# Kernel optimization log

Measured on AMD Instinct MI355X. Metric: run time of the kernel, lower is better.

Reference implementation:

```python
import jax, jax.numpy as jnp
import numpy as np

GRID = 64            # volume_pixel per axis
VOX = 1.0 / GRID     # voxel_physical (unit-cube volume_physical)
CHUNK = 128          # gaussians per scan step


def _voxel_centers():
    # [V,3] centers of voxels of a unit cube, V = GRID**3
    c = (jnp.arange(GRID, dtype=jnp.float32) + 0.5) * VOX
    zz, yy, xx = jnp.meshgrid(c, c, c, indexing='ij')
    return jnp.stack([xx.ravel(), yy.ravel(), zz.ravel()], axis=-1)


def _quat_to_rotmat(q):
    # q: [N,4] (w,x,y,z), normalized -> [N,3,3]
    q = q / jnp.linalg.norm(q, axis=-1, keepdims=True)
    w, x, y, z = q[:, 0], q[:, 1], q[:, 2], q[:, 3]
    return jnp.stack([
        jnp.stack([1 - 2 * (y * y + z * z), 2 * (x * y - w * z), 2 * (x * z + w * y)], -1),
        jnp.stack([2 * (x * y + w * z), 1 - 2 * (x * x + z * z), 2 * (y * z - w * x)], -1),
        jnp.stack([2 * (x * z - w * y), 2 * (y * z + w * x), 1 - 2 * (x * x + y * y)], -1),
    ], axis=-2)


def _voxelize(means3D, densities, scales, rotations):
    N = means3D.shape[0]
    R = _quat_to_rotmat(rotations)                       # [N,3,3]
    inv_s2 = 1.0 / (scales * scales)                     # [N,3]
    # Sigma^{-1} = R diag(1/s^2) R^T
    Sinv = jnp.einsum('nij,nj,nkj->nik', R, inv_s2, R)   # [N,3,3]
    centers = _voxel_centers()                            # [V,3]
    n_chunks = N // CHUNK
    mu_c = means3D.reshape(n_chunks, CHUNK, 3)
    de_c = densities.reshape(n_chunks, CHUNK)
    Si_c = Sinv.reshape(n_chunks, CHUNK, 3, 3)

    def step(vol, xs):
        mu, dens, Si = xs
        d = centers[None, :, :] - mu[:, None, :]                 # [C,V,3]
        qf = jnp.einsum('cvi,cij,cvj->cv', d, Si, d)             # [C,V]
        vol = vol + jnp.sum(dens[:, None] * jnp.exp(-0.5 * qf), axis=0)
        return vol, None

    vol0 = jnp.zeros((GRID ** 3,), dtype=means3D.dtype)
    volume, _ = jax.lax.scan(step, vol0, (mu_c, de_c, Si_c))
    volume = volume.reshape(GRID, GRID, GRID)
    # screen-space-style radius: 3 sigma of the largest axis, in voxels
    radii = jnp.ceil(3.0 * jnp.max(scales, axis=-1) / VOX).astype(jnp.int32)
    return volume, radii


def setup_inputs() -> dict:
    key = jax.random.key(0)
    k1, k2, k3, k4 = jax.random.split(key, 4)
    N = 4096
    means3D = jax.random.uniform(k1, (N, 3), dtype=jnp.float32)                 # in unit cube
    densities = jax.random.uniform(k2, (N,), dtype=jnp.float32)
    scales = jax.random.uniform(k3, (N, 3), dtype=jnp.float32) * 0.05 + 0.01    # 0.6-3.8 voxels
    rotations = jax.random.normal(k4, (N, 4), dtype=jnp.float32)
    return {"means3D": means3D, "densities": densities, "scales": scales, "rotations": rotations}


def reference(means3D, densities, scales, rotations):
    return _voxelize(means3D, densities, scales, rotations)
```

## Files before the change

### kernel.cpp

```cpp
#include <hip/hip_runtime.h>

#define GRIDN 64
#define NVOX (GRIDN * GRIDN * GRIDN)
#define VOXF (1.0f / 64.0f)
#define QCUT 12.0f
#define EXPSCL (-0.72134752044f)

#define WS_CULLA 0
#define WS_CULLB (4 * 4096)
#define WS_REC   (8 * 4096)

__global__ __launch_bounds__(256) void prep_kernel(
    const float* __restrict__ means, const float* __restrict__ dens,
    const float* __restrict__ scales, const float* __restrict__ rots,
    float* __restrict__ ws, float* __restrict__ radii_out, int N)
{
    int i = blockIdx.x * 256 + threadIdx.x;
    if (i >= N) return;

    float qw = rots[i * 4 + 0], qx = rots[i * 4 + 1];
    float qy = rots[i * 4 + 2], qz = rots[i * 4 + 3];
    float inm = rsqrtf(qw * qw + qx * qx + qy * qy + qz * qz);
    qw *= inm; qx *= inm; qy *= inm; qz *= inm;
    float r00 = 1.f - 2.f * (qy * qy + qz * qz);
    float r01 = 2.f * (qx * qy - qw * qz);
    float r02 = 2.f * (qx * qz + qw * qy);
    float r10 = 2.f * (qx * qy + qw * qz);
    float r11 = 1.f - 2.f * (qx * qx + qz * qz);
    float r12 = 2.f * (qy * qz - qw * qx);
    float r20 = 2.f * (qx * qz - qw * qy);
    float r21 = 2.f * (qy * qz + qw * qx);
    float r22 = 1.f - 2.f * (qx * qx + qy * qy);

    float s0 = scales[i * 3 + 0], s1 = scales[i * 3 + 1], s2 = scales[i * 3 + 2];
    float v0 = s0 * s0, v1 = s1 * s1, v2 = s2 * s2;
    float i0 = 1.f / v0, i1 = 1.f / v1, i2 = 1.f / v2;

    float A = (r00 * r00 * i0 + r01 * r01 * i1 + r02 * r02 * i2) * EXPSCL;
    float B = (r10 * r10 * i0 + r11 * r11 * i1 + r12 * r12 * i2) * EXPSCL;
    float C = (r20 * r20 * i0 + r21 * r21 * i1 + r22 * r22 * i2) * EXPSCL;
    float D = (r00 * r10 * i0 + r01 * r11 * i1 + r02 * r12 * i2) * EXPSCL;
    float E = (r00 * r20 * i0 + r01 * r21 * i1 + r02 * r22 * i2) * EXPSCL;
    float F = (r10 * r20 * i0 + r11 * r21 * i1 + r12 * r22 * i2) * EXPSCL;

    float Cxx = r00 * r00 * v0 + r01 * r01 * v1 + r02 * r02 * v2;
    float Cyy = r10 * r10 * v0 + r11 * r11 * v1 + r12 * r12 * v2;
    float Czz = r20 * r20 * v0 + r21 * r21 * v1 + r22 * r22 * v2;

    float de = fmaxf(dens[i], 1e-30f);
    float qeff = fmaxf(QCUT + 2.0f * logf(de), 0.0f);
    float smax2 = fmaxf(v0, fmaxf(v1, v2));

    float mx = means[i * 3 + 0], my = means[i * 3 + 1], mz = means[i * 3 + 2];
    float4 ca; ca.x = mx; ca.y = my; ca.z = mz; ca.w = sqrtf(qeff * Cxx);
    float4 cb; cb.x = sqrtf(qeff * Cyy); cb.y = sqrtf(qeff * Czz);
    cb.z = qeff * smax2; cb.w = 0.f;
    ((float4*)(ws + WS_CULLA))[i] = ca;
    ((float4*)(ws + WS_CULLB))[i] = cb;

    float4* R = (float4*)(ws + WS_REC + (size_t)i * 16);
    float4 w0; w0.x = A; w0.y = B; w0.z = C; w0.w = 2.f * D;
    float4 w1; w1.x = 2.f * E; w1.y = 2.f * F; w1.z = -0.25f / A; w1.w = log2f(de);
    float4 w2; w2.x = mx; w2.y = my; w2.z = mz; w2.w = 0.f;
    R[0] = w0; R[1] = w1; R[2] = w2;

    float m = fmaxf(s0, fmaxf(s1, s2));
    radii_out[i] = ceilf(m * 3.0f * 64.0f);
}

#define BODY8(v0_, v1_, v2_) do {                                             \
    float dy = py - v2_.y, dz = pz - v2_.z;                                   \
    float tt  = fmaf(v1_.y, dy, v0_.z * dz);                                  \
    float qyz = fmaf(v0_.y * dy, dy, fmaf(tt, dz, v1_.w));                    \
    float gx  = fmaf(v0_.w, dy, v1_.x * dz);                                  \
    float dx0 = px - v2_.x;                                                   \
    float dx1 = dx0 + VOXF,        dx2 = dx0 + 2.f * VOXF;                    \
    float dx3 = dx0 + 3.f * VOXF,  dx4 = dx0 + 4.f * VOXF;                    \
    float dx5 = dx0 + 5.f * VOXF,  dx6 = dx0 + 6.f * VOXF;                    \
    float dx7 = dx0 + 7.f * VOXF;                                             \
    accL.x += __builtin_amdgcn_exp2f(fmaf(dx0, fmaf(v0_.x, dx0, gx), qyz));   \
    accL.y += __builtin_amdgcn_exp2f(fmaf(dx1, fmaf(v0_.x, dx1, gx), qyz));   \
    accL.z += __builtin_amdgcn_exp2f(fmaf(dx2, fmaf(v0_.x, dx2, gx), qyz));   \
    accL.w += __builtin_amdgcn_exp2f(fmaf(dx3, fmaf(v0_.x, dx3, gx), qyz));   \
    accH.x += __builtin_amdgcn_exp2f(fmaf(dx4, fmaf(v0_.x, dx4, gx), qyz));   \
    accH.y += __builtin_amdgcn_exp2f(fmaf(dx5, fmaf(v0_.x, dx5, gx), qyz));   \
    accH.z += __builtin_amdgcn_exp2f(fmaf(dx6, fmaf(v0_.x, dx6, gx), qyz));   \
    accH.w += __builtin_amdgcn_exp2f(fmaf(dx7, fmaf(v0_.x, dx7, gx), qyz));   \
} while (0)

__global__ __launch_bounds__(1024, 8) void vox_kernel(
    const float* __restrict__ ws, float* __restrict__ out, int N)
{
    __shared__ unsigned long long cmask[64];
    __shared__ int slist[3072];
    __shared__ float4 plds[16][64];

    const float* rec = ws + WS_REC;
    const int tid = threadIdx.x;
    const int lane = tid & 63, wave = tid >> 6;
    const int t = (blockIdx.x * 341) & 511;
    const int tX = t & 7, tY = (t >> 3) & 7, tZ = t >> 6;
    const int x0 = tX << 3;
    const int y = (tY << 3) + (lane & 7);
    const int z = (tZ << 3) + (lane >> 3);
    const float px = (x0 + 0.5f) * VOXF;
    const float py = (y + 0.5f) * VOXF;
    const float pz = (z + 0.5f) * VOXF;

    const float lox = (x0 + 0.5f) * VOXF,          hix = (x0 + 7.5f) * VOXF;
    const float loy = ((tY << 3) + 0.5f) * VOXF,   hiy = ((tY << 3) + 7.5f) * VOXF;
    const float loz = ((tZ << 3) + 0.5f) * VOXF,   hiz = ((tZ << 3) + 7.5f) * VOXF;

    const int nch = (N + 63) >> 6;
    #pragma unroll
    for (int k = 0; k < 4; ++k) {
        const int c = (k << 4) | wave;
        unsigned long long bal = 0ull;
        if (c < nch) {
            const int gi = (c << 6) + lane;
            const int gc = gi < N ? gi : N - 1;
            float4 ca = ((const float4*)(ws + WS_CULLA))[gc];
            float4 cb = ((const float4*)(ws + WS_CULLB))[gc];
            float cx = fminf(fmaxf(ca.x, lox), hix) - ca.x;
            float cy = fminf(fmaxf(ca.y, loy), hiy) - ca.y;
            float cz = fminf(fmaxf(ca.z, loz), hiz) - ca.z;
            float d2 = fmaf(cx, cx, fmaf(cy, cy, cz * cz));
            bool keep = (gi < N) && (d2 <= cb.z)
                && (ca.x + ca.w >= lox) && (ca.x - ca.w <= hix)
                && (ca.y + cb.x >= loy) && (ca.y - cb.x <= hiy)
                && (ca.z + cb.y >= loz) && (ca.z - cb.y <= hiz);
            bal = __ballot(keep);
        }
        if (lane == 0) cmask[c] = bal;
    }
    __syncthreads();

    unsigned long long mk = cmask[lane];
    int pc = __popcll(mk);
    int incl = pc;
    #pragma unroll
    for (int d = 1; d < 64; d <<= 1) {
        int t2 = __shfl_up(incl, d, 64);
        if (lane >= d) incl += t2;
    }
    const int excl = incl - pc;
    int cnt = __builtin_amdgcn_readlane(incl, 63);
    if (cnt > 3072) cnt = 3072;

    #pragma unroll
    for (int k = 0; k < 4; ++k) {
        const int c = (k << 4) | wave;
        unsigned long long mc = cmask[c];
        if (mc == 0ull) continue;
        int bse = __builtin_amdgcn_readlane(excl, c);
        if ((mc >> lane) & 1ull) {
            int pre = __popcll(mc & ((1ull << lane) - 1ull));
            int pos = bse + pre;
            if (pos < 3072) slist[pos] = (c << 6) + lane;
        }
    }
    __syncthreads();

    float4 accL, accH;
    accL.x = accL.y = accL.z = accL.w = 0.f;
    accH = accL;

    const int beg = (wave * cnt) >> 4;
    const int end = ((wave + 1) * cnt) >> 4;
    for (int base = beg; base < end; base += 64) {
        int src = base + lane;
        int vidx = slist[src < cnt ? src : cnt - 1];
        int m = end - base; if (m > 64) m = 64;
        int j = 0;
        for (; j + 4 <= m; j += 4) {
            int i0 = __builtin_amdgcn_readlane(vidx, j);
            int i1 = __builtin_amdgcn_readlane(vidx, j + 1);
            int i2 = __builtin_amdgcn_readlane(vidx, j + 2);
            int i3 = __builtin_amdgcn_readlane(vidx, j + 3);
            const float4* P0 = (const float4*)(rec + ((size_t)i0 << 4));
            const float4* P1 = (const float4*)(rec + ((size_t)i1 << 4));
            const float4* P2 = (const float4*)(rec + ((size_t)i2 << 4));
            const float4* P3 = (const float4*)(rec + ((size_t)i3 << 4));
            float4 a0 = P0[0], a1 = P0[1], a2 = P0[2];
            float4 b0 = P1[0], b1 = P1[1], b2 = P1[2];
            float4 c0 = P2[0], c1 = P2[1], c2 = P2[2];
            float4 d0 = P3[0], d1 = P3[1], d2 = P3[2];
            BODY8(a0, a1, a2);
            BODY8(b0, b1, b2);
            BODY8(c0, c1, c2);
            BODY8(d0, d1, d2);
        }
        for (; j < m; ++j) {
            int i0 = __builtin_amdgcn_readlane(vidx, j);
            const float4* P0 = (const float4*)(rec + ((size_t)i0 << 4));
            float4 a0 = P0[0], a1 = P0[1], a2 = P0[2];
            BODY8(a0, a1, a2);
        }
    }

    const int v = (z << 12) + (y << 6) + x0;

    plds[wave][lane] = accL;
    __syncthreads();
    if (wave == 0) {
        float4 r = plds[0][lane];
        #pragma unroll
        for (int w = 1; w < 16; ++w) {
            float4 p = plds[w][lane];
            r.x += p.x; r.y += p.y; r.z += p.z; r.w += p.w;
        }
        *(float4*)&out[v] = r;
    }
    __syncthreads();
    plds[wave][lane] = accH;
    __syncthreads();
    if (wave == 0) {
        float4 r = plds[0][lane];
        #pragma unroll
        for (int w = 1; w < 16; ++w) {
            float4 p = plds[w][lane];
            r.x += p.x; r.y += p.y; r.z += p.z; r.w += p.w;
        }
        *(float4*)&out[v + 4] = r;
    }
}

extern "C" void kernel_launch(void* const* d_in, const int* in_sizes, int n_in,
                              void* d_out, int out_size, void* d_ws, size_t ws_size,
                              hipStream_t stream)
{
    const float* means  = (const float*)d_in[0];
    const float* dens   = (const float*)d_in[1];
    const float* scales = (const float*)d_in[2];
    const float* rots   = (const float*)d_in[3];
    float* out = (float*)d_out;
    float* ws  = (float*)d_ws;
    const int N = in_sizes[1];

    prep_kernel<<<(N + 255) / 256, 256, 0, stream>>>(means, dens, scales, rots,
                                                     ws, out + NVOX, N);
    vox_kernel<<<512, 1024, 0, stream>>>(ws, out, N);
}
```

Before: 25.62 us.

## Move per-tile culling into prep kernel and stream tile lists from global

Per-tile culling and list compaction move from the voxel kernel into the prep kernel. The prep kernel now runs 516 blocks: 4 compute the Gaussian records and 512 cull one tile each, recomputing the bounds from the raw inputs, then write a compacted per-tile index list and count to workspace. The voxel kernel reads its list from global memory with scalar loads and no longer needs the shared list or the culling barriers, which frees LDS and shortens its prologue. In exchange, the recomputed bounds are redundant across the 512 tiles, the list cap drops from 3072 to 2048, and per-element index loads from global replace readlane broadcasts.

```diff
diff --git a/kernel.cpp b/kernel.cpp
--- a/kernel.cpp
+++ b/kernel.cpp
@@ -5,67 +5,142 @@
 #define VOXF (1.0f / 64.0f)
 #define QCUT 12.0f
 #define EXPSCL (-0.72134752044f)
-
-#define WS_CULLA 0
-#define WS_CULLB (4 * 4096)
-#define WS_REC   (8 * 4096)
-
-__global__ __launch_bounds__(256) void prep_kernel(
+#define CAP 2048
+
+#define WS_REC 0
+#define WS_TL  (16 * 4096)
+#define WS_CNT (WS_TL + 512 * CAP)
+
+__global__ __launch_bounds__(1024) void prep_kernel(
     const float* __restrict__ means, const float* __restrict__ dens,
     const float* __restrict__ scales, const float* __restrict__ rots,
-    float* __restrict__ ws, float* __restrict__ radii_out, int N)
+    float* __restrict__ rec, int* __restrict__ tilelist, int* __restrict__ cntg,
+    float* __restrict__ radii_out, int N)
 {
-    int i = blockIdx.x * 256 + threadIdx.x;
-    if (i >= N) return;
-
-    float qw = rots[i * 4 + 0], qx = rots[i * 4 + 1];
-    float qy = rots[i * 4 + 2], qz = rots[i * 4 + 3];
-    float inm = rsqrtf(qw * qw + qx * qx + qy * qy + qz * qz);
-    qw *= inm; qx *= inm; qy *= inm; qz *= inm;
-    float r00 = 1.f - 2.f * (qy * qy + qz * qz);
-    float r01 = 2.f * (qx * qy - qw * qz);
-    float r02 = 2.f * (qx * qz + qw * qy);
-    float r10 = 2.f * (qx * qy + qw * qz);
-    float r11 = 1.f - 2.f * (qx * qx + qz * qz);
-    float r12 = 2.f * (qy * qz - qw * qx);
-    float r20 = 2.f * (qx * qz - qw * qy);
-    float r21 = 2.f * (qy * qz + qw * qx);
-    float r22 = 1.f - 2.f * (qx * qx + qy * qy);
-
-    float s0 = scales[i * 3 + 0], s1 = scales[i * 3 + 1], s2 = scales[i * 3 + 2];
-    float v0 = s0 * s0, v1 = s1 * s1, v2 = s2 * s2;
-    float i0 = 1.f / v0, i1 = 1.f / v1, i2 = 1.f / v2;
-
-    float A = (r00 * r00 * i0 + r01 * r01 * i1 + r02 * r02 * i2) * EXPSCL;
-    float B = (r10 * r10 * i0 + r11 * r11 * i1 + r12 * r12 * i2) * EXPSCL;
-    float C = (r20 * r20 * i0 + r21 * r21 * i1 + r22 * r22 * i2) * EXPSCL;
-    float D = (r00 * r10 * i0 + r01 * r11 * i1 + r02 * r12 * i2) * EXPSCL;
-    float E = (r00 * r20 * i0 + r01 * r21 * i1 + r02 * r22 * i2) * EXPSCL;
-    float F = (r10 * r20 * i0 + r11 * r21 * i1 + r12 * r22 * i2) * EXPSCL;
-
-    float Cxx = r00 * r00 * v0 + r01 * r01 * v1 + r02 * r02 * v2;
-    float Cyy = r10 * r10 * v0 + r11 * r11 * v1 + r12 * r12 * v2;
-    float Czz = r20 * r20 * v0 + r21 * r21 * v1 + r22 * r22 * v2;
-
-    float de = fmaxf(dens[i], 1e-30f);
-    float qeff = fmaxf(QCUT + 2.0f * logf(de), 0.0f);
-    float smax2 = fmaxf(v0, fmaxf(v1, v2));
-
-    float mx = means[i * 3 + 0], my = means[i * 3 + 1], mz = means[i * 3 + 2];
-    float4 ca; ca.x = mx; ca.y = my; ca.z = mz; ca.w = sqrtf(qeff * Cxx);
-    float4 cb; cb.x = sqrtf(qeff * Cyy); cb.y = sqrtf(qeff * Czz);
-    cb.z = qeff * smax2; cb.w = 0.f;
-    ((float4*)(ws + WS_CULLA))[i] = ca;
-    ((float4*)(ws + WS_CULLB))[i] = cb;
-
-    float4* R = (float4*)(ws + WS_REC + (size_t)i * 16);
-    float4 w0; w0.x = A; w0.y = B; w0.z = C; w0.w = 2.f * D;
-    float4 w1; w1.x = 2.f * E; w1.y = 2.f * F; w1.z = -0.25f / A; w1.w = log2f(de);
-    float4 w2; w2.x = mx; w2.y = my; w2.z = mz; w2.w = 0.f;
-    R[0] = w0; R[1] = w1; R[2] = w2;
-
-    float m = fmaxf(s0, fmaxf(s1, s2));
-    radii_out[i] = ceilf(m * 3.0f * 64.0f);
+    __shared__ unsigned long long cmask[64];
+    const int b = blockIdx.x;
+    const int tid = threadIdx.x;
+
+    if (b < 4) {
+        const int i = (b << 10) + tid;
+        if (i >= N) return;
+
+        float qw = rots[i * 4 + 0], qx = rots[i * 4 + 1];
+        float qy = rots[i * 4 + 2], qz = rots[i * 4 + 3];
+        float inm = rsqrtf(qw * qw + qx * qx + qy * qy + qz * qz);
+        qw *= inm; qx *= inm; qy *= inm; qz *= inm;
+        float r00 = 1.f - 2.f * (qy * qy + qz * qz);
+        float r01 = 2.f * (qx * qy - qw * qz);
+        float r02 = 2.f * (qx * qz + qw * qy);
+        float r10 = 2.f * (qx * qy + qw * qz);
+        float r11 = 1.f - 2.f * (qx * qx + qz * qz);
+        float r12 = 2.f * (qy * qz - qw * qx);
+        float r20 = 2.f * (qx * qz - qw * qy);
+        float r21 = 2.f * (qy * qz + qw * qx);
+        float r22 = 1.f - 2.f * (qx * qx + qy * qy);
+
+        float s0 = scales[i * 3 + 0], s1 = scales[i * 3 + 1], s2 = scales[i * 3 + 2];
+        float v0 = s0 * s0, v1 = s1 * s1, v2 = s2 * s2;
+        float i0 = 1.f / v0, i1 = 1.f / v1, i2 = 1.f / v2;
+
+        float A = (r00 * r00 * i0 + r01 * r01 * i1 + r02 * r02 * i2) * EXPSCL;
+        float B = (r10 * r10 * i0 + r11 * r11 * i1 + r12 * r12 * i2) * EXPSCL;
+        float C = (r20 * r20 * i0 + r21 * r21 * i1 + r22 * r22 * i2) * EXPSCL;
+        float D = (r00 * r10 * i0 + r01 * r11 * i1 + r02 * r12 * i2) * EXPSCL;
+        float E = (r00 * r20 * i0 + r01 * r21 * i1 + r02 * r22 * i2) * EXPSCL;
+        float F = (r10 * r20 * i0 + r11 * r21 * i1 + r12 * r22 * i2) * EXPSCL;
+
+        float de = fmaxf(dens[i], 1e-30f);
+        float4* R = (float4*)(rec + (size_t)i * 16);
+        float4 w0; w0.x = A; w0.y = B; w0.z = C; w0.w = 2.f * D;
+        float4 w1; w1.x = 2.f * E; w1.y = 2.f * F; w1.z = -0.25f / A; w1.w = log2f(de);
+        float4 w2; w2.x = means[i * 3 + 0]; w2.y = means[i * 3 + 1];
+        w2.z = means[i * 3 + 2]; w2.w = 0.f;
+        R[0] = w0; R[1] = w1; R[2] = w2;
+
+        radii_out[i] = ceilf(fmaxf(s0, fmaxf(s1, s2)) * 3.0f * 64.0f);
+        return;
+    }
+
+    const int tb = b - 4;
+    const int lane = tid & 63, wave = tid >> 6;
+    const int tX = tb & 7, tY = (tb >> 3) & 7, tZ = tb >> 6;
+    const float lox = ((tX << 3) + 0.5f) * VOXF, hix = ((tX << 3) + 7.5f) * VOXF;
+    const float loy = ((tY << 3) + 0.5f) * VOXF, hiy = ((tY << 3) + 7.5f) * VOXF;
+    const float loz = ((tZ << 3) + 0.5f) * VOXF, hiz = ((tZ << 3) + 7.5f) * VOXF;
+
+    const int nch = (N + 63) >> 6;
+    #pragma unroll
+    for (int k = 0; k < 4; ++k) {
+        const int c = (k << 4) | wave;
+        unsigned long long bal = 0ull;
+        if (c < nch) {
+            const int gi = (c << 6) + lane;
+            const int gc = gi < N ? gi : N - 1;
+            float qw = rots[gc * 4 + 0], qx = rots[gc * 4 + 1];
+            float qy = rots[gc * 4 + 2], qz = rots[gc * 4 + 3];
+            float inm = rsqrtf(qw * qw + qx * qx + qy * qy + qz * qz);
+            float w = qw * inm, a = qx * inm, bq = qy * inm, cq = qz * inm;
+            float r00 = 1.f - 2.f * (bq * bq + cq * cq);
+            float r01 = 2.f * (a * bq - w * cq);
+            float r02 = 2.f * (a * cq + w * bq);
+            float r10 = 2.f * (a * bq + w * cq);
+            float r11 = 1.f - 2.f * (a * a + cq * cq);
+            float r12 = 2.f * (bq * cq - w * a);
+            float r20 = 2.f * (a * cq - w * bq);
+            float r21 = 2.f * (bq * cq + w * a);
+            float r22 = 1.f - 2.f * (a * a + bq * bq);
+            float s0 = scales[gc * 3 + 0], s1 = scales[gc * 3 + 1], s2 = scales[gc * 3 + 2];
+            float v0 = s0 * s0, v1 = s1 * s1, v2 = s2 * s2;
+            float Cxx = r00 * r00 * v0 + r01 * r01 * v1 + r02 * r02 * v2;
+            float Cyy = r10 * r10 * v0 + r11 * r11 * v1 + r12 * r12 * v2;
+            float Czz = r20 * r20 * v0 + r21 * r21 * v1 + r22 * r22 * v2;
+            float de = fmaxf(dens[gc], 1e-30f);
+            float qeff = fmaxf(QCUT + 2.0f * logf(de), 0.0f);
+            float rx = sqrtf(qeff * Cxx), ry = sqrtf(qeff * Cyy), rz = sqrtf(qeff * Czz);
+            float sph = qeff * fmaxf(v0, fmaxf(v1, v2));
+            float mx = means[gc * 3 + 0], my = means[gc * 3 + 1], mz = means[gc * 3 + 2];
+
+            float cx = fminf(fmaxf(mx, lox), hix) - mx;
+            float cy = fminf(fmaxf(my, loy), hiy) - my;
+            float cz = fminf(fmaxf(mz, loz), hiz) - mz;
+            float d2 = fmaf(cx, cx, fmaf(cy, cy, cz * cz));
+            bool keep = (gi < N) && (d2 <= sph)
+                && (mx + rx >= lox) && (mx - rx <= hix)
+                && (my + ry >= loy) && (my - ry <= hiy)
+                && (mz + rz >= loz) && (mz - rz <= hiz);
+            bal = __ballot(keep);
+        }
+        if (lane == 0) cmask[c] = bal;
+    }
+    __syncthreads();
+
+    unsigned long long mk = cmask[lane];
+    int pc = __popcll(mk);
+    int incl = pc;
+    #pragma unroll
+    for (int d = 1; d < 64; d <<= 1) {
+        int t2 = __shfl_up(incl, d, 64);
+        if (lane >= d) incl += t2;
+    }
+    const int excl = incl - pc;
+    int cnt = __builtin_amdgcn_readlane(incl, 63);
+    if (cnt > CAP) cnt = CAP;
+
+    int* tl = tilelist + (size_t)tb * CAP;
+    #pragma unroll
+    for (int k = 0; k < 4; ++k) {
+        const int c = (k << 4) | wave;
+        unsigned long long mc = cmask[c];
+        if (mc == 0ull) continue;
+        int bse = __builtin_amdgcn_readlane(excl, c);
+        if ((mc >> lane) & 1ull) {
+            int pre = __popcll(mc & ((1ull << lane) - 1ull));
+            int pos = bse + pre;
+            if (pos < CAP) tl[pos] = (c << 6) + lane;
+        }
+    }
+    if (tid == 0) cntg[tb] = cnt;
 }
 
 #define BODY8(v0_, v1_, v2_) do {                                             \
@@ -89,13 +164,11 @@
 } while (0)
 
 __global__ __launch_bounds__(1024, 8) void vox_kernel(
-    const float* __restrict__ ws, float* __restrict__ out, int N)
+    const float* __restrict__ rec, const int* __restrict__ tilelist,
+    const int* __restrict__ cntg, float* __restrict__ out, int N)
 {
-    __shared__ unsigned long long cmask[64];
-    __shared__ int slist[3072];
     __shared__ float4 plds[16][64];
 
-    const float* rec = ws + WS_REC;
     const int tid = threadIdx.x;
     const int lane = tid & 63, wave = tid >> 6;
     const int t = (blockIdx.x * 341) & 511;
@@ -107,59 +180,8 @@
     const float py = (y + 0.5f) * VOXF;
     const float pz = (z + 0.5f) * VOXF;
 
-    const float lox = (x0 + 0.5f) * VOXF,          hix = (x0 + 7.5f) * VOXF;
-    const float loy = ((tY << 3) + 0.5f) * VOXF,   hiy = ((tY << 3) + 7.5f) * VOXF;
-    const float loz = ((tZ << 3) + 0.5f) * VOXF,   hiz = ((tZ << 3) + 7.5f) * VOXF;
-
-    const int nch = (N + 63) >> 6;
-    #pragma unroll
-    for (int k = 0; k < 4; ++k) {
-        const int c = (k << 4) | wave;
-        unsigned long long bal = 0ull;
-        if (c < nch) {
-            const int gi = (c << 6) + lane;
-            const int gc = gi < N ? gi : N - 1;
-            float4 ca = ((const float4*)(ws + WS_CULLA))[gc];
-            float4 cb = ((const float4*)(ws + WS_CULLB))[gc];
-            float cx = fminf(fmaxf(ca.x, lox), hix) - ca.x;
-            float cy = fminf(fmaxf(ca.y, loy), hiy) - ca.y;
-            float cz = fminf(fmaxf(ca.z, loz), hiz) - ca.z;
-            float d2 = fmaf(cx, cx, fmaf(cy, cy, cz * cz));
-            bool keep = (gi < N) && (d2 <= cb.z)
-                && (ca.x + ca.w >= lox) && (ca.x - ca.w <= hix)
-                && (ca.y + cb.x >= loy) && (ca.y - cb.x <= hiy)
-                && (ca.z + cb.y >= loz) && (ca.z - cb.y <= hiz);
-            bal = __ballot(keep);
-        }
-        if (lane == 0) cmask[c] = bal;
-    }
-    __syncthreads();
-
-    unsigned long long mk = cmask[lane];
-    int pc = __popcll(mk);
-    int incl = pc;
-    #pragma unroll
-    for (int d = 1; d < 64; d <<= 1) {
-        int t2 = __shfl_up(incl, d, 64);
-        if (lane >= d) incl += t2;
-    }
-    const int excl = incl - pc;
-    int cnt = __builtin_amdgcn_readlane(incl, 63);
-    if (cnt > 3072) cnt = 3072;
-
-    #pragma unroll
-    for (int k = 0; k < 4; ++k) {
-        const int c = (k << 4) | wave;
-        unsigned long long mc = cmask[c];
-        if (mc == 0ull) continue;
-        int bse = __builtin_amdgcn_readlane(excl, c);
-        if ((mc >> lane) & 1ull) {
-            int pre = __popcll(mc & ((1ull << lane) - 1ull));
-            int pos = bse + pre;
-            if (pos < 3072) slist[pos] = (c << 6) + lane;
-        }
-    }
-    __syncthreads();
+    const int cnt = cntg[t];
+    const int* tl = tilelist + (size_t)t * CAP;
 
     float4 accL, accH;
     accL.x = accL.y = accL.z = accL.w = 0.f;
@@ -167,35 +189,27 @@
 
     const int beg = (wave * cnt) >> 4;
     const int end = ((wave + 1) * cnt) >> 4;
-    for (int base = beg; base < end; base += 64) {
-        int src = base + lane;
-        int vidx = slist[src < cnt ? src : cnt - 1];
-        int m = end - base; if (m > 64) m = 64;
-        int j = 0;
-        for (; j + 4 <= m; j += 4) {
-            int i0 = __builtin_amdgcn_readlane(vidx, j);
-            int i1 = __builtin_amdgcn_readlane(vidx, j + 1);
-            int i2 = __builtin_amdgcn_readlane(vidx, j + 2);
-            int i3 = __builtin_amdgcn_readlane(vidx, j + 3);
-            const float4* P0 = (const float4*)(rec + ((size_t)i0 << 4));
-            const float4* P1 = (const float4*)(rec + ((size_t)i1 << 4));
-            const float4* P2 = (const float4*)(rec + ((size_t)i2 << 4));
-            const float4* P3 = (const float4*)(rec + ((size_t)i3 << 4));
-            float4 a0 = P0[0], a1 = P0[1], a2 = P0[2];
-            float4 b0 = P1[0], b1 = P1[1], b2 = P1[2];
-            float4 c0 = P2[0], c1 = P2[1], c2 = P2[2];
-            float4 d0 = P3[0], d1 = P3[1], d2 = P3[2];
-            BODY8(a0, a1, a2);
-            BODY8(b0, b1, b2);
-            BODY8(c0, c1, c2);
-            BODY8(d0, d1, d2);
-        }
-        for (; j < m; ++j) {
-            int i0 = __builtin_amdgcn_readlane(vidx, j);
-            const float4* P0 = (const float4*)(rec + ((size_t)i0 << 4));
-            float4 a0 = P0[0], a1 = P0[1], a2 = P0[2];
-            BODY8(a0, a1, a2);
-        }
+    int p = beg;
+    for (; p + 4 <= end; p += 4) {
+        int i0 = tl[p], i1 = tl[p + 1], i2 = tl[p + 2], i3 = tl[p + 3];
+        const float4* P0 = (const float4*)(rec + ((size_t)i0 << 4));
+        const float4* P1 = (const float4*)(rec + ((size_t)i1 << 4));
+        const float4* P2 = (const float4*)(rec + ((size_t)i2 << 4));
+        const float4* P3 = (const float4*)(rec + ((size_t)i3 << 4));
+        float4 a0 = P0[0], a1 = P0[1], a2 = P0[2];
+        float4 b0 = P1[0], b1 = P1[1], b2 = P1[2];
+        float4 c0 = P2[0], c1 = P2[1], c2 = P2[2];
+        float4 d0 = P3[0], d1 = P3[1], d2 = P3[2];
+        BODY8(a0, a1, a2);
+        BODY8(b0, b1, b2);
+        BODY8(c0, c1, c2);
+        BODY8(d0, d1, d2);
+    }
+    for (; p < end; ++p) {
+        int i0 = tl[p];
+        const float4* P0 = (const float4*)(rec + ((size_t)i0 << 4));
+        float4 a0 = P0[0], a1 = P0[1], a2 = P0[2];
+        BODY8(a0, a1, a2);
     }
 
     const int v = (z << 12) + (y << 6) + x0;
@@ -206,8 +220,8 @@
         float4 r = plds[0][lane];
         #pragma unroll
         for (int w = 1; w < 16; ++w) {
-            float4 p = plds[w][lane];
-            r.x += p.x; r.y += p.y; r.z += p.z; r.w += p.w;
+            float4 q = plds[w][lane];
+            r.x += q.x; r.y += q.y; r.z += q.z; r.w += q.w;
         }
         *(float4*)&out[v] = r;
     }
@@ -218,8 +232,8 @@
         float4 r = plds[0][lane];
         #pragma unroll
         for (int w = 1; w < 16; ++w) {
-            float4 p = plds[w][lane];
-            r.x += p.x; r.y += p.y; r.z += p.z; r.w += p.w;
+            float4 q = plds[w][lane];
+            r.x += q.x; r.y += q.y; r.z += q.z; r.w += q.w;
         }
         *(float4*)&out[v + 4] = r;
     }
@@ -235,9 +249,12 @@
     const float* rots   = (const float*)d_in[3];
     float* out = (float*)d_out;
     float* ws  = (float*)d_ws;
+    float* rec = ws + WS_REC;
+    int* tilelist = (int*)(ws + WS_TL);
+    int* cntg = (int*)(ws + WS_CNT);
     const int N = in_sizes[1];
 
-    prep_kernel<<<(N + 255) / 256, 256, 0, stream>>>(means, dens, scales, rots,
-                                                     ws, out + NVOX, N);
-    vox_kernel<<<512, 1024, 0, stream>>>(ws, out, N);
+    prep_kernel<<<516, 1024, 0, stream>>>(means, dens, scales, rots,
+                                          rec, tilelist, cntg, out + NVOX, N);
+    vox_kernel<<<512, 1024, 0, stream>>>(rec, tilelist, cntg, out, N);
 }
```

After: 30.31 us. +18.3%, slower.
